# Optimization experiments

Hardware: AMD Instinct MI355X
Metric: run time of the kernel (lower is better)

Reference implementation:

```python
import jax, jax.numpy as jnp
import numpy as np

QUANT_BLOCK = 32  # GGUF Q4_0-style block size
QUANT_ZERO = 8.0  # 4-bit codes are offset-binary around 8


def setup_inputs() -> dict:
    key = jax.random.key(0)
    k_x, k_q, k_s, k_up, k_dn, k_b = jax.random.split(key, 6)
    O, I, R = 4096, 4096, 16
    T = 2048  # tokens (batch*seq)
    x = jax.random.normal(k_x, (T, I), dtype=jnp.float32)
    # quantized 4-bit codes stored unpacked as int32 in [0, 16)
    q = jax.random.randint(k_q, (O, I), 0, 16, dtype=jnp.int32)
    # per-block scales (small positive, like real GGUF d values)
    scales = jax.random.uniform(k_s, (O, I // QUANT_BLOCK), dtype=jnp.float32) * 0.05
    lora_up = jax.random.normal(k_up, (O, R), dtype=jnp.float32) * 0.02
    lora_down = jax.random.normal(k_dn, (R, I), dtype=jnp.float32) * 0.02
    alpha = jnp.ones((), dtype=jnp.float32)
    bias = jax.random.normal(k_b, (O,), dtype=jnp.float32)
    return {"x": x, "q": q, "scales": scales, "lora_up": lora_up,
            "lora_down": lora_down, "alpha": alpha, "bias": bias}


def _dequant(q, scales):
    # q: [O, I] int codes; scales: [O, I/BLOCK] per-block scale
    O, I = q.shape
    qf = q.reshape(O, I // QUANT_BLOCK, QUANT_BLOCK).astype(scales.dtype)
    w = (qf - QUANT_ZERO) * scales[:, :, None]  # [O, I/B, B]
    return w.reshape(O, I)


def reference(x, q, scales, lora_up, lora_down, alpha, bias):
    # on-the-fly dequant (GGMLLayer.get_weight -> dequantize_tensor)
    W = _dequant(q, scales)  # [O, I]
    # LoRA patch apply (ray_calculate_weight): W += alpha * up @ down
    W = W + alpha * jnp.einsum('or,ri->oi', lora_up, lora_down)
    # linear forward: y = x @ W^T + b
    return jnp.einsum('ti,oi->to', x, W) + bias
```

## Files before the change

kernel.cpp:

```cpp
#include <hip/hip_runtime.h>
#include <hip/hip_bf16.h>
#include <stdint.h>

#define T_DIM 2048
#define I_DIM 4096
#define O_DIM 4096
#define R_DIM 16
#define QBLK  32

typedef __bf16 bf16x8 __attribute__((ext_vector_type(8)));
typedef float  floatx4 __attribute__((ext_vector_type(4)));
typedef unsigned short ushort_t;

#define AS1 __attribute__((address_space(1)))
#define AS3 __attribute__((address_space(3)))

__device__ __forceinline__ ushort_t f2bf(float f) {
  unsigned u = __float_as_uint(f);
  u += 0x7FFFu + ((u >> 16) & 1u);
  return (ushort_t)(u >> 16);
}

__device__ __forceinline__ float dot4(float4 a, float4 b) {
  return a.x * b.x + a.y * b.y + a.z * b.z + a.w * b.w;
}

__global__ __launch_bounds__(256) void k_prep(const float* __restrict__ x,
                                              const int* __restrict__ q,
                                              const float* __restrict__ scales,
                                              const float* __restrict__ down,
                                              const float* __restrict__ alphap,
                                              ushort_t* __restrict__ xb,
                                              ushort_t* __restrict__ wb,
                                              float* __restrict__ xd) {
  __shared__ float ds[16 * 512];
  const int b = blockIdx.x, tid = threadIdx.x;

  if (b >= 256 && b < 4352) {
    int idx = (b - 256) * 256 + tid;
    const float4* xp = (const float4*)x;
    float4 a = xp[idx * 2], c = xp[idx * 2 + 1];
    union { ushort_t u[8]; uint4 v; } r;
    r.u[0] = f2bf(a.x); r.u[1] = f2bf(a.y); r.u[2] = f2bf(a.z); r.u[3] = f2bf(a.w);
    r.u[4] = f2bf(c.x); r.u[5] = f2bf(c.y); r.u[6] = f2bf(c.z); r.u[7] = f2bf(c.w);
    ((uint4*)xb)[idx] = r.v;
    return;
  }
  if (b >= 4352) {
    int idx = (b - 4352) * 256 + tid;
    int o  = idx >> 9;
    int i0 = (idx & 511) * 8;
    float s = scales[o * (I_DIM / QBLK) + (i0 >> 5)];
    const int4* qp = (const int4*)(q + (size_t)o * I_DIM + i0);
    int4 q0 = qp[0], q1 = qp[1];
    union { ushort_t u[8]; uint4 v; } r;
    r.u[0] = f2bf((float)(q0.x - 8) * s); r.u[1] = f2bf((float)(q0.y - 8) * s);
    r.u[2] = f2bf((float)(q0.z - 8) * s); r.u[3] = f2bf((float)(q0.w - 8) * s);
    r.u[4] = f2bf((float)(q1.x - 8) * s); r.u[5] = f2bf((float)(q1.y - 8) * s);
    r.u[6] = f2bf((float)(q1.z - 8) * s); r.u[7] = f2bf((float)(q1.w - 8) * s);
    ((uint4*)wb)[idx] = r.v;
    return;
  }
  {
    const int blk = b;
    const int tl = tid >> 5, s = tid & 31;
    const int t = blk * 8 + tl;
    float acc[16];
#pragma unroll
    for (int r = 0; r < 16; ++r) acc[r] = 0.f;
    for (int c = 0; c < 8; ++c) {
      const int ib = c * 512;
      __syncthreads();
#pragma unroll
      for (int j = 0; j < 8; ++j) {
        int e = j * 256 + tid;
        int r = e >> 7, col = e & 127;
        ((float4*)ds)[e] = ((const float4*)(down + (size_t)r * I_DIM + ib))[col];
      }
      __syncthreads();
#pragma unroll
      for (int j = 0; j < 4; ++j) {
        float4 xv = ((const float4*)(x + (size_t)t * I_DIM + ib))[s + 32 * j];
#pragma unroll
        for (int r = 0; r < 16; ++r) {
          float4 dv = ((const float4*)ds)[r * 128 + s + 32 * j];
          acc[r] += dot4(xv, dv);
        }
      }
    }
    const float al = alphap[0];
#pragma unroll
    for (int r = 0; r < 16; ++r) {
      float v = acc[r];
      v += __shfl_down(v, 16, 32);
      v += __shfl_down(v, 8, 32);
      v += __shfl_down(v, 4, 32);
      v += __shfl_down(v, 2, 32);
      v += __shfl_down(v, 1, 32);
      if (s == 0) xd[t * 16 + r] = v * al;
    }
  }
}


#define BK 32
#define NT (I_DIM / BK)
#define TILE_E (128 * BK)

__device__ __forceinline__ bf16x8 lds_read16(unsigned addr) {
  bf16x8 d;
  asm volatile("ds_read_b128 %0, %1" : "=v"(d) : "v"(addr));
  return d;
}

__device__ __forceinline__ void stage2(const ushort_t* __restrict__ g,
                                       ushort_t* lds0, int wv, int lane) {
#pragma unroll
  for (int it = 0; it < 2; ++it) {
    const int seg_base = it * 256 + wv * 64;
    const int seg = seg_base + lane;
    const int r  = seg >> 2;
    const int cg = (seg & 3) ^ ((r + (r >> 2)) & 3);
    __builtin_amdgcn_global_load_lds(
        (const AS1 char*)(g + (size_t)r * I_DIM + cg * 8),
        (AS3 char*)(lds0 + seg_base * 8), 16, 0, 0);
  }
}

template<int VM, bool STG>
__device__ __forceinline__ void ktile(unsigned aB, unsigned bB,
                                      ushort_t* Ast, ushort_t* Bst,
                                      const ushort_t* ga, const ushort_t* gb,
                                      floatx4 (&acc)[4][4], int wv, int lane) {
  const int quad = lane >> 4, m16 = lane & 15;
  const int wm = wv >> 1, wn = wv & 1;
  bf16x8 af[4], bfr[4];
#pragma unroll
  for (int im = 0; im < 4; ++im) {
    const int m = wm * 64 + im * 16 + m16;
    af[im] = lds_read16(aB + (unsigned)(m * 64 + ((quad ^ ((m + (m >> 2)) & 3)) << 4)));
  }
#pragma unroll
  for (int in_ = 0; in_ < 4; ++in_) {
    const int n = wn * 64 + in_ * 16 + m16;
    bfr[in_] = lds_read16(bB + (unsigned)(n * 64 + ((quad ^ ((n + (n >> 2)) & 3)) << 4)));
  }
  if constexpr (STG) { stage2(ga, Ast, wv, lane); stage2(gb, Bst, wv, lane); }
  __builtin_amdgcn_s_barrier();
  asm volatile("s_waitcnt lgkmcnt(0)" ::: "memory");
  __builtin_amdgcn_sched_barrier(0);
  __builtin_amdgcn_s_setprio(1);
#pragma unroll
  for (int im = 0; im < 4; ++im)
#pragma unroll
    for (int in_ = 0; in_ < 4; ++in_)
      acc[im][in_] = __builtin_amdgcn_mfma_f32_16x16x32_bf16(
          af[im], bfr[in_], acc[im][in_], 0, 0, 0);
  __builtin_amdgcn_s_setprio(0);
  if constexpr (VM == 8)      asm volatile("s_waitcnt vmcnt(8)" ::: "memory");
  else if constexpr (VM == 4) asm volatile("s_waitcnt vmcnt(4)" ::: "memory");
  else if constexpr (VM == 0) asm volatile("s_waitcnt vmcnt(0)" ::: "memory");
  if constexpr (VM >= 0) __builtin_amdgcn_sched_barrier(0);
  __builtin_amdgcn_s_barrier();
}

__global__ __launch_bounds__(256, 2) void k_gemm(const ushort_t* __restrict__ xb,
                                                 const ushort_t* __restrict__ wb,
                                                 const float* __restrict__ bias,
                                                 const float* __restrict__ xd,
                                                 const float* __restrict__ up,
                                                 float* __restrict__ y) {
  __shared__ __align__(16) ushort_t As[4][TILE_E];
  __shared__ __align__(16) ushort_t Bs[4][TILE_E];

  const int tid = threadIdx.x;
  const int wv = tid >> 6, lane = tid & 63;

  const int id = blockIdx.x;
  const int sid = (id & 7) * 64 + (id >> 3);
  const int bx = sid >> 4;
  const int by = sid & 15;
  const int oT = bx * 128, tT = by * 128;

  const ushort_t* ap = xb + (size_t)tT * I_DIM;
  const ushort_t* bp = wb + (size_t)oT * I_DIM;

  const unsigned asB = (unsigned)(uintptr_t)(AS3 ushort_t*)&As[0][0];
  const unsigned bsB = (unsigned)(uintptr_t)(AS3 ushort_t*)&Bs[0][0];

  floatx4 acc[4][4] = {};

#pragma unroll
  for (int t = 0; t < 3; ++t) {
    stage2(ap + t * BK, As[t], wv, lane);
    stage2(bp + t * BK, Bs[t], wv, lane);
  }
  asm volatile("s_waitcnt vmcnt(8)" ::: "memory");
  __builtin_amdgcn_sched_barrier(0);
  __builtin_amdgcn_s_barrier();

  for (int kt = 0; kt < NT - 3; ++kt) {
    const int cur = kt & 3, st = (kt + 3) & 3;
    ktile<8, true>(asB + cur * (TILE_E * 2), bsB + cur * (TILE_E * 2),
                   As[st], Bs[st],
                   ap + (size_t)(kt + 3) * BK, bp + (size_t)(kt + 3) * BK,
                   acc, wv, lane);
  }
  ktile<4, false>(asB + ((NT - 3) & 3) * (TILE_E * 2), bsB + ((NT - 3) & 3) * (TILE_E * 2),
                  nullptr, nullptr, nullptr, nullptr, acc, wv, lane);
  ktile<0, false>(asB + ((NT - 2) & 3) * (TILE_E * 2), bsB + ((NT - 2) & 3) * (TILE_E * 2),
                  nullptr, nullptr, nullptr, nullptr, acc, wv, lane);
  ktile<-1, false>(asB + ((NT - 1) & 3) * (TILE_E * 2), bsB + ((NT - 1) & 3) * (TILE_E * 2),
                   nullptr, nullptr, nullptr, nullptr, acc, wv, lane);

  const int quad = lane >> 4, m16 = lane & 15;
  const int wm = wv >> 1, wn = wv & 1;
#pragma unroll
  for (int im = 0; im < 4; ++im) {
#pragma unroll
    for (int reg = 0; reg < 4; ++reg) {
      const int t = tT + wm * 64 + im * 16 + quad * 4 + reg;
      const float4* xr = (const float4*)(xd + t * 16);
      float4 x0 = xr[0], x1 = xr[1], x2 = xr[2], x3 = xr[3];
#pragma unroll
      for (int in_ = 0; in_ < 4; ++in_) {
        const int o = oT + wn * 64 + in_ * 16 + m16;
        const float4* ur = (const float4*)(up + (size_t)o * R_DIM);
        float lv = dot4(x0, ur[0]) + dot4(x1, ur[1]) +
                   dot4(x2, ur[2]) + dot4(x3, ur[3]);
        y[(size_t)t * O_DIM + o] = acc[im][in_][reg] + lv + bias[o];
      }
    }
  }
}

extern "C" void kernel_launch(void* const* d_in, const int* in_sizes, int n_in,
                              void* d_out, int out_size, void* d_ws, size_t ws_size,
                              hipStream_t stream) {
  const float* x      = (const float*)d_in[0];
  const int*   q      = (const int*)d_in[1];
  const float* scales = (const float*)d_in[2];
  const float* up     = (const float*)d_in[3];
  const float* down   = (const float*)d_in[4];
  const float* alpha  = (const float*)d_in[5];
  const float* bias   = (const float*)d_in[6];
  float* y = (float*)d_out;

  ushort_t* xb = (ushort_t*)d_ws;
  ushort_t* wb = (ushort_t*)((char*)d_ws + (size_t)T_DIM * I_DIM * 2);
  float*    xd = (float*)((char*)d_ws + (size_t)T_DIM * I_DIM * 2 + (size_t)O_DIM * I_DIM * 2);

  hipLaunchKernelGGL(k_prep, dim3(256 + 4096 + 8192), dim3(256), 0, stream,
                     x, q, scales, down, alpha, xb, wb, xd);
  hipLaunchKernelGGL(k_gemm, dim3((O_DIM / 128) * (T_DIM / 128)), dim3(256), 0, stream,
                     xb, wb, bias, xd, up, y);
}
```

Measured before the change: 454.1 us.

## Replace pipelined multi-stage GEMM with simple single-buffer BK=64 loop

Removes the 4-stage asynchronous global-to-LDS pipeline with manual waitcnt and barrier scheduling. In its place is a straightforward loop that loads a 64-wide K tile into a single LDS buffer, syncs, and runs the MFMAs. It also drops the XCD-aware block index swizzle in favour of a 2D grid. In the prep kernel, lora_down is read from global memory instead of being staged in shared memory. This simplifies the code and reduces LDS use, but loses the overlap of memory loads with compute and the L2 locality from the swizzle.

```diff
diff --git a/kernel.cpp b/kernel.cpp
--- a/kernel.cpp
+++ b/kernel.cpp
@@ -33,7 +33,6 @@
                                               ushort_t* __restrict__ xb,
                                               ushort_t* __restrict__ wb,
                                               float* __restrict__ xd) {
-  __shared__ float ds[16 * 512];
   const int b = blockIdx.x, tid = threadIdx.x;
 
   if (b >= 256 && b < 4352) {
@@ -70,20 +69,12 @@
     for (int r = 0; r < 16; ++r) acc[r] = 0.f;
     for (int c = 0; c < 8; ++c) {
       const int ib = c * 512;
-      __syncthreads();
-#pragma unroll
-      for (int j = 0; j < 8; ++j) {
-        int e = j * 256 + tid;
-        int r = e >> 7, col = e & 127;
-        ((float4*)ds)[e] = ((const float4*)(down + (size_t)r * I_DIM + ib))[col];
-      }
-      __syncthreads();
 #pragma unroll
       for (int j = 0; j < 4; ++j) {
         float4 xv = ((const float4*)(x + (size_t)t * I_DIM + ib))[s + 32 * j];
 #pragma unroll
         for (int r = 0; r < 16; ++r) {
-          float4 dv = ((const float4*)ds)[r * 128 + s + 32 * j];
+          float4 dv = ((const float4*)(down + (size_t)r * I_DIM + ib))[s + 32 * j];
           acc[r] += dot4(xv, dv);
         }
       }
@@ -103,118 +94,74 @@
 }
 
 
-#define BK 32
-#define NT (I_DIM / BK)
-#define TILE_E (128 * BK)
-
-__device__ __forceinline__ bf16x8 lds_read16(unsigned addr) {
-  bf16x8 d;
-  asm volatile("ds_read_b128 %0, %1" : "=v"(d) : "v"(addr));
-  return d;
-}
-
-__device__ __forceinline__ void stage2(const ushort_t* __restrict__ g,
-                                       ushort_t* lds0, int wv, int lane) {
-#pragma unroll
-  for (int it = 0; it < 2; ++it) {
-    const int seg_base = it * 256 + wv * 64;
-    const int seg = seg_base + lane;
-    const int r  = seg >> 2;
-    const int cg = (seg & 3) ^ ((r + (r >> 2)) & 3);
-    __builtin_amdgcn_global_load_lds(
-        (const AS1 char*)(g + (size_t)r * I_DIM + cg * 8),
-        (AS3 char*)(lds0 + seg_base * 8), 16, 0, 0);
-  }
-}
-
-template<int VM, bool STG>
-__device__ __forceinline__ void ktile(unsigned aB, unsigned bB,
-                                      ushort_t* Ast, ushort_t* Bst,
-                                      const ushort_t* ga, const ushort_t* gb,
-                                      floatx4 (&acc)[4][4], int wv, int lane) {
+__global__ __launch_bounds__(256) void k_gemm(const ushort_t* __restrict__ xb,
+                                              const ushort_t* __restrict__ wb,
+                                              const float* __restrict__ bias,
+                                              const float* __restrict__ xd,
+                                              const float* __restrict__ up,
+                                              float* __restrict__ y) {
+  __shared__ __align__(16) ushort_t As[128 * 64];
+  __shared__ __align__(16) ushort_t Bs[128 * 64];
+
+  const int tid = threadIdx.x;
+  const int wv = tid >> 6, lane = tid & 63;
   const int quad = lane >> 4, m16 = lane & 15;
   const int wm = wv >> 1, wn = wv & 1;
-  bf16x8 af[4], bfr[4];
-#pragma unroll
-  for (int im = 0; im < 4; ++im) {
-    const int m = wm * 64 + im * 16 + m16;
-    af[im] = lds_read16(aB + (unsigned)(m * 64 + ((quad ^ ((m + (m >> 2)) & 3)) << 4)));
-  }
-#pragma unroll
-  for (int in_ = 0; in_ < 4; ++in_) {
-    const int n = wn * 64 + in_ * 16 + m16;
-    bfr[in_] = lds_read16(bB + (unsigned)(n * 64 + ((quad ^ ((n + (n >> 2)) & 3)) << 4)));
-  }
-  if constexpr (STG) { stage2(ga, Ast, wv, lane); stage2(gb, Bst, wv, lane); }
-  __builtin_amdgcn_s_barrier();
-  asm volatile("s_waitcnt lgkmcnt(0)" ::: "memory");
-  __builtin_amdgcn_sched_barrier(0);
-  __builtin_amdgcn_s_setprio(1);
-#pragma unroll
-  for (int im = 0; im < 4; ++im)
-#pragma unroll
-    for (int in_ = 0; in_ < 4; ++in_)
-      acc[im][in_] = __builtin_amdgcn_mfma_f32_16x16x32_bf16(
-          af[im], bfr[in_], acc[im][in_], 0, 0, 0);
-  __builtin_amdgcn_s_setprio(0);
-  if constexpr (VM == 8)      asm volatile("s_waitcnt vmcnt(8)" ::: "memory");
-  else if constexpr (VM == 4) asm volatile("s_waitcnt vmcnt(4)" ::: "memory");
-  else if constexpr (VM == 0) asm volatile("s_waitcnt vmcnt(0)" ::: "memory");
-  if constexpr (VM >= 0) __builtin_amdgcn_sched_barrier(0);
-  __builtin_amdgcn_s_barrier();
-}
-
-__global__ __launch_bounds__(256, 2) void k_gemm(const ushort_t* __restrict__ xb,
-                                                 const ushort_t* __restrict__ wb,
-                                                 const float* __restrict__ bias,
-                                                 const float* __restrict__ xd,
-                                                 const float* __restrict__ up,
-                                                 float* __restrict__ y) {
-  __shared__ __align__(16) ushort_t As[4][TILE_E];
-  __shared__ __align__(16) ushort_t Bs[4][TILE_E];
-
-  const int tid = threadIdx.x;
-  const int wv = tid >> 6, lane = tid & 63;
-
-  const int id = blockIdx.x;
-  const int sid = (id & 7) * 64 + (id >> 3);
-  const int bx = sid >> 4;
-  const int by = sid & 15;
-  const int oT = bx * 128, tT = by * 128;
-
+
+  const int oT = blockIdx.x * 128, tT = blockIdx.y * 128;
   const ushort_t* ap = xb + (size_t)tT * I_DIM;
   const ushort_t* bp = wb + (size_t)oT * I_DIM;
 
-  const unsigned asB = (unsigned)(uintptr_t)(AS3 ushort_t*)&As[0][0];
-  const unsigned bsB = (unsigned)(uintptr_t)(AS3 ushort_t*)&Bs[0][0];
-
   floatx4 acc[4][4] = {};
 
-#pragma unroll
-  for (int t = 0; t < 3; ++t) {
-    stage2(ap + t * BK, As[t], wv, lane);
-    stage2(bp + t * BK, Bs[t], wv, lane);
-  }
-  asm volatile("s_waitcnt vmcnt(8)" ::: "memory");
-  __builtin_amdgcn_sched_barrier(0);
-  __builtin_amdgcn_s_barrier();
-
-  for (int kt = 0; kt < NT - 3; ++kt) {
-    const int cur = kt & 3, st = (kt + 3) & 3;
-    ktile<8, true>(asB + cur * (TILE_E * 2), bsB + cur * (TILE_E * 2),
-                   As[st], Bs[st],
-                   ap + (size_t)(kt + 3) * BK, bp + (size_t)(kt + 3) * BK,
-                   acc, wv, lane);
-  }
-  ktile<4, false>(asB + ((NT - 3) & 3) * (TILE_E * 2), bsB + ((NT - 3) & 3) * (TILE_E * 2),
-                  nullptr, nullptr, nullptr, nullptr, acc, wv, lane);
-  ktile<0, false>(asB + ((NT - 2) & 3) * (TILE_E * 2), bsB + ((NT - 2) & 3) * (TILE_E * 2),
-                  nullptr, nullptr, nullptr, nullptr, acc, wv, lane);
-  ktile<-1, false>(asB + ((NT - 1) & 3) * (TILE_E * 2), bsB + ((NT - 1) & 3) * (TILE_E * 2),
-                   nullptr, nullptr, nullptr, nullptr, acc, wv, lane);
-
-  const int quad = lane >> 4, m16 = lane & 15;
-  const int wm = wv >> 1, wn = wv & 1;
+  for (int kt = 0; kt < I_DIM / 64; ++kt) {
+    const int k0 = kt * 64;
+#pragma unroll
+    for (int it = 0; it < 4; ++it) {
+      const int seg_base = it * 256 + wv * 64;
+      const int seg = seg_base + lane;
+      const int r  = seg >> 3;
+      const int cg = (seg & 7) ^ (r & 7);
+      __builtin_amdgcn_global_load_lds(
+          (const AS1 char*)(ap + (size_t)r * I_DIM + k0 + cg * 8),
+          (AS3 char*)(As + seg_base * 8), 16, 0, 0);
+    }
+#pragma unroll
+    for (int it = 0; it < 4; ++it) {
+      const int seg_base = it * 256 + wv * 64;
+      const int seg = seg_base + lane;
+      const int r  = seg >> 3;
+      const int cg = (seg & 7) ^ (r & 7);
+      __builtin_amdgcn_global_load_lds(
+          (const AS1 char*)(bp + (size_t)r * I_DIM + k0 + cg * 8),
+          (AS3 char*)(Bs + seg_base * 8), 16, 0, 0);
+    }
+    __syncthreads();
+
+#pragma unroll
+    for (int ks2 = 0; ks2 < 2; ++ks2) {
+      const int c = ks2 * 4 + quad;
+      bf16x8 af[4], bfr[4];
+#pragma unroll
+      for (int im = 0; im < 4; ++im) {
+        const int m = wm * 64 + im * 16 + m16;
+        af[im] = *(const bf16x8*)(As + (m * 8 + (c ^ (m & 7))) * 8);
+      }
+#pragma unroll
+      for (int in_ = 0; in_ < 4; ++in_) {
+        const int n = wn * 64 + in_ * 16 + m16;
+        bfr[in_] = *(const bf16x8*)(Bs + (n * 8 + (c ^ (n & 7))) * 8);
+      }
+#pragma unroll
+      for (int im = 0; im < 4; ++im)
+#pragma unroll
+        for (int in_ = 0; in_ < 4; ++in_)
+          acc[im][in_] = __builtin_amdgcn_mfma_f32_16x16x32_bf16(
+              af[im], bfr[in_], acc[im][in_], 0, 0, 0);
+    }
+    __syncthreads();
+  }
+
 #pragma unroll
   for (int im = 0; im < 4; ++im) {
 #pragma unroll
@@ -252,6 +199,6 @@
 
   hipLaunchKernelGGL(k_prep, dim3(256 + 4096 + 8192), dim3(256), 0, stream,
                      x, q, scales, down, alpha, xb, wb, xd);
-  hipLaunchKernelGGL(k_gemm, dim3((O_DIM / 128) * (T_DIM / 128)), dim3(256), 0, stream,
+  hipLaunchKernelGGL(k_gemm, dim3(O_DIM / 128, T_DIM / 128), dim3(256), 0, stream,
                      xb, wb, bias, xd, up, y);
 }
```

Result: slower. 575.4 us (+26.7%).

## Enlarge GEMM tile to 128x256 with BK=64, 8 waves, triple buffering

Applied to the files above, without the earlier changes.

The GEMM now uses 512-thread blocks, each computing a 128x256 output tile with K-step 64 and a three-stage LDS ring instead of a four-stage one. LDS fragment reads are split into two halves so MFMAs can start before all reads complete. The tile-order swizzle is replaced by a plain 2D grid. The prep kernel is also split into a streaming convert/dequant kernel and a separate LoRA x@down kernel. The aim is more data reuse per LDS byte and fewer loop iterations, at the cost of more LDS per block (~144KB), which may limit occupancy, and one extra launch.

```diff
diff --git a/kernel.cpp b/kernel.cpp
--- a/kernel.cpp
+++ b/kernel.cpp
@@ -25,19 +25,14 @@
   return a.x * b.x + a.y * b.y + a.z * b.z + a.w * b.w;
 }
 
-__global__ __launch_bounds__(256) void k_prep(const float* __restrict__ x,
-                                              const int* __restrict__ q,
-                                              const float* __restrict__ scales,
-                                              const float* __restrict__ down,
-                                              const float* __restrict__ alphap,
-                                              ushort_t* __restrict__ xb,
-                                              ushort_t* __restrict__ wb,
-                                              float* __restrict__ xd) {
-  __shared__ float ds[16 * 512];
+__global__ __launch_bounds__(256) void k_stream(const float* __restrict__ x,
+                                                const int* __restrict__ q,
+                                                const float* __restrict__ scales,
+                                                ushort_t* __restrict__ xb,
+                                                ushort_t* __restrict__ wb) {
   const int b = blockIdx.x, tid = threadIdx.x;
-
-  if (b >= 256 && b < 4352) {
-    int idx = (b - 256) * 256 + tid;
+  if (b < 4096) {
+    int idx = b * 256 + tid;
     const float4* xp = (const float4*)x;
     float4 a = xp[idx * 2], c = xp[idx * 2 + 1];
     union { ushort_t u[8]; uint4 v; } r;
@@ -46,8 +41,8 @@
     ((uint4*)xb)[idx] = r.v;
     return;
   }
-  if (b >= 4352) {
-    int idx = (b - 4352) * 256 + tid;
+  {
+    int idx = (b - 4096) * 256 + tid;
     int o  = idx >> 9;
     int i0 = (idx & 511) * 8;
     float s = scales[o * (I_DIM / QBLK) + (i0 >> 5)];
@@ -59,53 +54,58 @@
     r.u[4] = f2bf((float)(q1.x - 8) * s); r.u[5] = f2bf((float)(q1.y - 8) * s);
     r.u[6] = f2bf((float)(q1.z - 8) * s); r.u[7] = f2bf((float)(q1.w - 8) * s);
     ((uint4*)wb)[idx] = r.v;
-    return;
-  }
-  {
-    const int blk = b;
-    const int tl = tid >> 5, s = tid & 31;
-    const int t = blk * 8 + tl;
-    float acc[16];
-#pragma unroll
-    for (int r = 0; r < 16; ++r) acc[r] = 0.f;
-    for (int c = 0; c < 8; ++c) {
-      const int ib = c * 512;
-      __syncthreads();
-#pragma unroll
-      for (int j = 0; j < 8; ++j) {
-        int e = j * 256 + tid;
-        int r = e >> 7, col = e & 127;
-        ((float4*)ds)[e] = ((const float4*)(down + (size_t)r * I_DIM + ib))[col];
-      }
-      __syncthreads();
-#pragma unroll
-      for (int j = 0; j < 4; ++j) {
-        float4 xv = ((const float4*)(x + (size_t)t * I_DIM + ib))[s + 32 * j];
-#pragma unroll
-        for (int r = 0; r < 16; ++r) {
-          float4 dv = ((const float4*)ds)[r * 128 + s + 32 * j];
-          acc[r] += dot4(xv, dv);
-        }
+  }
+}
+
+__global__ __launch_bounds__(256) void k_xd(const float* __restrict__ x,
+                                            const float* __restrict__ down,
+                                            const float* __restrict__ alphap,
+                                            float* __restrict__ xd) {
+  __shared__ float ds[16 * 512];
+  const int b = blockIdx.x, tid = threadIdx.x;
+  const int tl = tid >> 5, s = tid & 31;
+  const int t = b * 8 + tl;
+  float acc[16];
+#pragma unroll
+  for (int r = 0; r < 16; ++r) acc[r] = 0.f;
+  for (int c = 0; c < 8; ++c) {
+    const int ib = c * 512;
+    __syncthreads();
+#pragma unroll
+    for (int j = 0; j < 8; ++j) {
+      int e = j * 256 + tid;
+      int r = e >> 7, col = e & 127;
+      ((float4*)ds)[e] = ((const float4*)(down + (size_t)r * I_DIM + ib))[col];
+    }
+    __syncthreads();
+#pragma unroll
+    for (int j = 0; j < 4; ++j) {
+      float4 xv = ((const float4*)(x + (size_t)t * I_DIM + ib))[s + 32 * j];
+#pragma unroll
+      for (int r = 0; r < 16; ++r) {
+        float4 dv = ((const float4*)ds)[r * 128 + s + 32 * j];
+        acc[r] += dot4(xv, dv);
       }
     }
-    const float al = alphap[0];
-#pragma unroll
-    for (int r = 0; r < 16; ++r) {
-      float v = acc[r];
-      v += __shfl_down(v, 16, 32);
-      v += __shfl_down(v, 8, 32);
-      v += __shfl_down(v, 4, 32);
-      v += __shfl_down(v, 2, 32);
-      v += __shfl_down(v, 1, 32);
-      if (s == 0) xd[t * 16 + r] = v * al;
-    }
-  }
-}
-
-
-#define BK 32
+  }
+  const float al = alphap[0];
+#pragma unroll
+  for (int r = 0; r < 16; ++r) {
+    float v = acc[r];
+    v += __shfl_down(v, 16, 32);
+    v += __shfl_down(v, 8, 32);
+    v += __shfl_down(v, 4, 32);
+    v += __shfl_down(v, 2, 32);
+    v += __shfl_down(v, 1, 32);
+    if (s == 0) xd[t * 16 + r] = v * al;
+  }
+}
+
+
+#define BK 64
 #define NT (I_DIM / BK)
-#define TILE_E (128 * BK)
+#define ASZ (128 * BK)
+#define BSZ (256 * BK)
 
 __device__ __forceinline__ bf16x8 lds_read16(unsigned addr) {
   bf16x8 d;
@@ -113,17 +113,24 @@
   return d;
 }
 
-__device__ __forceinline__ void stage2(const ushort_t* __restrict__ g,
-                                       ushort_t* lds0, int wv, int lane) {
+__device__ __forceinline__ void stage6(const ushort_t* __restrict__ ga,
+                                       const ushort_t* __restrict__ gb,
+                                       ushort_t* Ast, ushort_t* Bst, int tid) {
 #pragma unroll
   for (int it = 0; it < 2; ++it) {
-    const int seg_base = it * 256 + wv * 64;
-    const int seg = seg_base + lane;
-    const int r  = seg >> 2;
-    const int cg = (seg & 3) ^ ((r + (r >> 2)) & 3);
+    const int seg = it * 512 + tid;
+    const int r = seg >> 3, cg = (seg & 7) ^ (r & 7);
     __builtin_amdgcn_global_load_lds(
-        (const AS1 char*)(g + (size_t)r * I_DIM + cg * 8),
-        (AS3 char*)(lds0 + seg_base * 8), 16, 0, 0);
+        (const AS1 char*)(ga + (size_t)r * I_DIM + cg * 8),
+        (AS3 char*)(Ast + (size_t)seg * 8), 16, 0, 0);
+  }
+#pragma unroll
+  for (int it = 0; it < 4; ++it) {
+    const int seg = it * 512 + tid;
+    const int r = seg >> 3, cg = (seg & 7) ^ (r & 7);
+    __builtin_amdgcn_global_load_lds(
+        (const AS1 char*)(gb + (size_t)r * I_DIM + cg * 8),
+        (AS3 char*)(Bst + (size_t)seg * 8), 16, 0, 0);
   }
 }
 
@@ -131,90 +138,99 @@
 __device__ __forceinline__ void ktile(unsigned aB, unsigned bB,
                                       ushort_t* Ast, ushort_t* Bst,
                                       const ushort_t* ga, const ushort_t* gb,
-                                      floatx4 (&acc)[4][4], int wv, int lane) {
+                                      floatx4 (&acc)[4][4], int tid) {
+  const int lane = tid & 63, wv = tid >> 6;
   const int quad = lane >> 4, m16 = lane & 15;
-  const int wm = wv >> 1, wn = wv & 1;
-  bf16x8 af[4], bfr[4];
-#pragma unroll
-  for (int im = 0; im < 4; ++im) {
-    const int m = wm * 64 + im * 16 + m16;
-    af[im] = lds_read16(aB + (unsigned)(m * 64 + ((quad ^ ((m + (m >> 2)) & 3)) << 4)));
-  }
-#pragma unroll
-  for (int in_ = 0; in_ < 4; ++in_) {
-    const int n = wn * 64 + in_ * 16 + m16;
-    bfr[in_] = lds_read16(bB + (unsigned)(n * 64 + ((quad ^ ((n + (n >> 2)) & 3)) << 4)));
-  }
-  if constexpr (STG) { stage2(ga, Ast, wv, lane); stage2(gb, Bst, wv, lane); }
-  __builtin_amdgcn_s_barrier();
+  const int wm = wv >> 2, wn = wv & 3;
+
+  if constexpr (STG) stage6(ga, gb, Ast, Bst, tid);
+
+  bf16x8 a0[4], b0[4], a1[4], b1[4];
+#pragma unroll
+  for (int i = 0; i < 4; ++i) {
+    const int m = wm * 64 + i * 16 + m16;
+    a0[i] = lds_read16(aB + (unsigned)((m * 8 + (quad ^ (m & 7))) * 16));
+  }
+#pragma unroll
+  for (int i = 0; i < 4; ++i) {
+    const int n = wn * 64 + i * 16 + m16;
+    b0[i] = lds_read16(bB + (unsigned)((n * 8 + (quad ^ (n & 7))) * 16));
+  }
+#pragma unroll
+  for (int i = 0; i < 4; ++i) {
+    const int m = wm * 64 + i * 16 + m16;
+    a1[i] = lds_read16(aB + (unsigned)((m * 8 + ((4 + quad) ^ (m & 7))) * 16));
+  }
+#pragma unroll
+  for (int i = 0; i < 4; ++i) {
+    const int n = wn * 64 + i * 16 + m16;
+    b1[i] = lds_read16(bB + (unsigned)((n * 8 + ((4 + quad) ^ (n & 7))) * 16));
+  }
+  asm volatile("s_waitcnt lgkmcnt(8)" ::: "memory");
+  __builtin_amdgcn_sched_barrier(0);
+  __builtin_amdgcn_s_setprio(1);
+#pragma unroll
+  for (int i = 0; i < 4; ++i)
+#pragma unroll
+    for (int j = 0; j < 4; ++j)
+      acc[i][j] = __builtin_amdgcn_mfma_f32_16x16x32_bf16(a0[i], b0[j], acc[i][j], 0, 0, 0);
+  __builtin_amdgcn_s_setprio(0);
   asm volatile("s_waitcnt lgkmcnt(0)" ::: "memory");
   __builtin_amdgcn_sched_barrier(0);
   __builtin_amdgcn_s_setprio(1);
 #pragma unroll
-  for (int im = 0; im < 4; ++im)
-#pragma unroll
-    for (int in_ = 0; in_ < 4; ++in_)
-      acc[im][in_] = __builtin_amdgcn_mfma_f32_16x16x32_bf16(
-          af[im], bfr[in_], acc[im][in_], 0, 0, 0);
+  for (int i = 0; i < 4; ++i)
+#pragma unroll
+    for (int j = 0; j < 4; ++j)
+      acc[i][j] = __builtin_amdgcn_mfma_f32_16x16x32_bf16(a1[i], b1[j], acc[i][j], 0, 0, 0);
   __builtin_amdgcn_s_setprio(0);
-  if constexpr (VM == 8)      asm volatile("s_waitcnt vmcnt(8)" ::: "memory");
-  else if constexpr (VM == 4) asm volatile("s_waitcnt vmcnt(4)" ::: "memory");
+  if constexpr (VM == 6)      asm volatile("s_waitcnt vmcnt(6)" ::: "memory");
   else if constexpr (VM == 0) asm volatile("s_waitcnt vmcnt(0)" ::: "memory");
   if constexpr (VM >= 0) __builtin_amdgcn_sched_barrier(0);
   __builtin_amdgcn_s_barrier();
 }
 
-__global__ __launch_bounds__(256, 2) void k_gemm(const ushort_t* __restrict__ xb,
+__global__ __launch_bounds__(512, 2) void k_gemm(const ushort_t* __restrict__ xb,
                                                  const ushort_t* __restrict__ wb,
                                                  const float* __restrict__ bias,
                                                  const float* __restrict__ xd,
                                                  const float* __restrict__ up,
                                                  float* __restrict__ y) {
-  __shared__ __align__(16) ushort_t As[4][TILE_E];
-  __shared__ __align__(16) ushort_t Bs[4][TILE_E];
+  __shared__ __align__(16) ushort_t As[3][ASZ];
+  __shared__ __align__(16) ushort_t Bs[3][BSZ];
 
   const int tid = threadIdx.x;
-  const int wv = tid >> 6, lane = tid & 63;
-
-  const int id = blockIdx.x;
-  const int sid = (id & 7) * 64 + (id >> 3);
-  const int bx = sid >> 4;
-  const int by = sid & 15;
-  const int oT = bx * 128, tT = by * 128;
-
+  const int oT = blockIdx.x * 256, tT = blockIdx.y * 128;
   const ushort_t* ap = xb + (size_t)tT * I_DIM;
   const ushort_t* bp = wb + (size_t)oT * I_DIM;
 
-  const unsigned asB = (unsigned)(uintptr_t)(AS3 ushort_t*)&As[0][0];
-  const unsigned bsB = (unsigned)(uintptr_t)(AS3 ushort_t*)&Bs[0][0];
+  const unsigned aL = (unsigned)(uintptr_t)(AS3 ushort_t*)&As[0][0];
+  const unsigned bL = (unsigned)(uintptr_t)(AS3 ushort_t*)&Bs[0][0];
+  const unsigned aS0 = aL, aS1 = aL + ASZ * 2, aS2 = aL + ASZ * 4;
+  const unsigned bS0 = bL, bS1 = bL + BSZ * 2, bS2 = bL + BSZ * 4;
 
   floatx4 acc[4][4] = {};
 
-#pragma unroll
-  for (int t = 0; t < 3; ++t) {
-    stage2(ap + t * BK, As[t], wv, lane);
-    stage2(bp + t * BK, Bs[t], wv, lane);
-  }
-  asm volatile("s_waitcnt vmcnt(8)" ::: "memory");
+  stage6(ap, bp, As[0], Bs[0], tid);
+  stage6(ap + BK, bp + BK, As[1], Bs[1], tid);
+  asm volatile("s_waitcnt vmcnt(6)" ::: "memory");
   __builtin_amdgcn_sched_barrier(0);
   __builtin_amdgcn_s_barrier();
 
-  for (int kt = 0; kt < NT - 3; ++kt) {
-    const int cur = kt & 3, st = (kt + 3) & 3;
-    ktile<8, true>(asB + cur * (TILE_E * 2), bsB + cur * (TILE_E * 2),
-                   As[st], Bs[st],
-                   ap + (size_t)(kt + 3) * BK, bp + (size_t)(kt + 3) * BK,
-                   acc, wv, lane);
-  }
-  ktile<4, false>(asB + ((NT - 3) & 3) * (TILE_E * 2), bsB + ((NT - 3) & 3) * (TILE_E * 2),
-                  nullptr, nullptr, nullptr, nullptr, acc, wv, lane);
-  ktile<0, false>(asB + ((NT - 2) & 3) * (TILE_E * 2), bsB + ((NT - 2) & 3) * (TILE_E * 2),
-                  nullptr, nullptr, nullptr, nullptr, acc, wv, lane);
-  ktile<-1, false>(asB + ((NT - 1) & 3) * (TILE_E * 2), bsB + ((NT - 1) & 3) * (TILE_E * 2),
-                   nullptr, nullptr, nullptr, nullptr, acc, wv, lane);
-
+  int kc = 2 * BK;
+  for (int g = 0; g < 20; ++g) {
+    ktile<6, true>(aS0, bS0, As[2], Bs[2], ap + kc, bp + kc, acc, tid); kc += BK;
+    ktile<6, true>(aS1, bS1, As[0], Bs[0], ap + kc, bp + kc, acc, tid); kc += BK;
+    ktile<6, true>(aS2, bS2, As[1], Bs[1], ap + kc, bp + kc, acc, tid); kc += BK;
+  }
+  ktile<6, true>(aS0, bS0, As[2], Bs[2], ap + kc, bp + kc, acc, tid); kc += BK;
+  ktile<6, true>(aS1, bS1, As[0], Bs[0], ap + kc, bp + kc, acc, tid);
+  ktile<0, false>(aS2, bS2, nullptr, nullptr, nullptr, nullptr, acc, tid);
+  ktile<-1, false>(aS0, bS0, nullptr, nullptr, nullptr, nullptr, acc, tid);
+
+  const int lane = tid & 63, wv = tid >> 6;
   const int quad = lane >> 4, m16 = lane & 15;
-  const int wm = wv >> 1, wn = wv & 1;
+  const int wm = wv >> 2, wn = wv & 3;
 #pragma unroll
   for (int im = 0; im < 4; ++im) {
 #pragma unroll
@@ -250,8 +266,9 @@
   ushort_t* wb = (ushort_t*)((char*)d_ws + (size_t)T_DIM * I_DIM * 2);
   float*    xd = (float*)((char*)d_ws + (size_t)T_DIM * I_DIM * 2 + (size_t)O_DIM * I_DIM * 2);
 
-  hipLaunchKernelGGL(k_prep, dim3(256 + 4096 + 8192), dim3(256), 0, stream,
-                     x, q, scales, down, alpha, xb, wb, xd);
-  hipLaunchKernelGGL(k_gemm, dim3((O_DIM / 128) * (T_DIM / 128)), dim3(256), 0, stream,
+  hipLaunchKernelGGL(k_stream, dim3(4096 + 8192), dim3(256), 0, stream,
+                     x, q, scales, xb, wb);
+  hipLaunchKernelGGL(k_xd, dim3(256), dim3(256), 0, stream, x, down, alpha, xd);
+  hipLaunchKernelGGL(k_gemm, dim3(O_DIM / 256, T_DIM / 128), dim3(512), 0, stream,
                      xb, wb, bias, xd, up, y);
 }
```

Result: faster. 435.3 us (-4.1%).
